# Performance work log

Hardware: AMD Instinct MI355X
Metric: run time of the kernel (lower is better)

The kernel has to match this reference:

```python
import jax, jax.numpy as jnp
import numpy as np

NUM_RELATIONS = 8
NUM_BASES = 4
IN_CH, HID, OUT_CH = 128, 64, 64
N_NODES, N_EDGES = 50000, 500000


def rgcn_conv(x, edge_src, edge_dst, edge_type, basis, comp, root, bias):
    """PyG RGCNConv with basis decomposition and per-relation mean aggregation.
    basis: [B, in, out], comp: [R, B], root: [in, out], bias: [out].
    W_r = sum_b comp[r, b] * basis[b]; msg_e = x[src_e] @ W_{type_e};
    aggregate mean over incoming edges per (node, relation), sum over relations,
    then add root transform and bias.
    """
    n = x.shape[0]
    out_dim = basis.shape[2]
    # Project once through all bases: [N, B, out]  (cheap: B=4)
    h = jnp.einsum('ni,bio->nbo', x, basis)
    # Per-edge message: contract gathered basis features with per-edge comp coeffs
    msg = jnp.einsum('eb,ebo->eo', comp[edge_type], h[edge_src])  # [E, out]
    # Mean aggregation per (dst, relation): segment id = dst*R + relation
    seg = edge_dst * NUM_RELATIONS + edge_type
    sums = jax.ops.segment_sum(msg, seg, num_segments=n * NUM_RELATIONS)
    cnt = jax.ops.segment_sum(jnp.ones((msg.shape[0], 1), msg.dtype), seg,
                              num_segments=n * NUM_RELATIONS)
    mean = sums / jnp.maximum(cnt, 1.0)
    agg = mean.reshape(n, NUM_RELATIONS, out_dim).sum(axis=1)
    return agg + x @ root + bias


def setup_inputs() -> dict:
    key = jax.random.key(0)
    ks = jax.random.split(key, 12)
    s1 = 1.0 / np.sqrt(IN_CH)
    s2 = 1.0 / np.sqrt(HID)
    return {
        'x': jax.random.normal(ks[0], (N_NODES, IN_CH), jnp.float32),
        'edge_index': jax.random.randint(ks[1], (2, N_EDGES), 0, N_NODES, jnp.int64),
        'edge_type': jax.random.randint(ks[2], (N_EDGES,), 0, NUM_RELATIONS, jnp.int64),
        'basis1': jax.random.normal(ks[3], (NUM_BASES, IN_CH, HID), jnp.float32) * s1,
        'comp1': jax.random.normal(ks[4], (NUM_RELATIONS, NUM_BASES), jnp.float32) * 0.5,
        'root1': jax.random.normal(ks[5], (IN_CH, HID), jnp.float32) * s1,
        'bias1': jnp.zeros((HID,), jnp.float32),
        'basis2': jax.random.normal(ks[6], (NUM_BASES, HID, OUT_CH), jnp.float32) * s2,
        'comp2': jax.random.normal(ks[7], (NUM_RELATIONS, NUM_BASES), jnp.float32) * 0.5,
        'root2': jax.random.normal(ks[8], (HID, OUT_CH), jnp.float32) * s2,
        'bias2': jnp.zeros((OUT_CH,), jnp.float32),
    }


def reference(x, edge_index, edge_type, basis1, comp1, root1, bias1,
              basis2, comp2, root2, bias2):
    src, dst = edge_index[0], edge_index[1]
    h = rgcn_conv(x, src, dst, edge_type, basis1, comp1, root1, bias1)
    h = jax.nn.relu(h)
    out = rgcn_conv(h, src, dst, edge_type, basis2, comp2, root2, bias2)
    return out
```

## Files before the change

### kernel.cpp

```cpp
#include <hip/hip_runtime.h>
#include <cstddef>

#define NREL 8
#define SCAN_TILE 4096

typedef __bf16 bf16x8 __attribute__((ext_vector_type(8)));
typedef float f32x4 __attribute__((ext_vector_type(4)));

__device__ __forceinline__ unsigned f2bf_u(float f) {
    unsigned u = __float_as_uint(f);
    u += 0x7FFFu + ((u >> 16) & 1u);
    return u >> 16;
}
__device__ __forceinline__ short f2bf(float f) { return (short)f2bf_u(f); }
__device__ __forceinline__ int pack2bf(float lo, float hi) {
    return (int)(f2bf_u(lo) | (f2bf_u(hi) << 16));
}
__device__ __forceinline__ float bfval(unsigned short g) {
    return __uint_as_float((unsigned)g << 16);
}

__global__ __launch_bounds__(256) void zero_kernel(int4* __restrict__ p, int n16,
                                                   int* __restrict__ offsN, int E)
{
    int i = blockIdx.x * 256 + threadIdx.x;
    if (i < n16) p[i] = make_int4(0, 0, 0, 0);
    if (i == 0) *offsN = E;
}

template<int K>
__device__ __forceinline__ void wfrag_body(const float* __restrict__ basis,
                                           const float* __restrict__ root,
                                           const float* __restrict__ comp,
                                           short* __restrict__ Wf, int tid)
{
    constexpr int NK = K / 32;
    int lane = tid & 63, slot = tid >> 6;
    int ks = slot % NK, t = slot / NK;
    int kg = lane >> 4, lr = lane & 15;
    int k0 = ks * 32 + kg * 8;
    union { short s[8]; int4 v; } u;
#pragma unroll
    for (int e = 0; e < 8; ++e) {
        int k = k0 + e;
        float v;
        if (t < 32) {
            int rr = t >> 2, ch = (t & 3) * 16 + lr;
            v = comp[rr * 4 + 0] * basis[((size_t)0 * K + k) * 64 + ch]
              + comp[rr * 4 + 1] * basis[((size_t)1 * K + k) * 64 + ch]
              + comp[rr * 4 + 2] * basis[((size_t)2 * K + k) * 64 + ch]
              + comp[rr * 4 + 3] * basis[((size_t)3 * K + k) * 64 + ch];
        } else {
            v = root[(size_t)k * 64 + (t - 32) * 16 + lr];
        }
        u.s[e] = f2bf(v);
    }
    *(int4*)(Wf + (size_t)tid * 8) = u.v;
}

__device__ __forceinline__ void afrag_body128(const float* __restrict__ x,
                                              short* __restrict__ xf, int N, int tid)
{
    int lane = tid & 63, slot = tid >> 6;
    int ks = slot & 3, rt = slot >> 2;
    int kg = lane >> 4, lr = lane & 15;
    int row = rt * 16 + lr, k = ks * 32 + kg * 8;
    union { short s[8]; int4 v; } u;
    if (row < N) {
        const float* xp = x + (size_t)row * 128 + k;
        float4 a = *(const float4*)xp;
        float4 b = *(const float4*)(xp + 4);
        u.s[0] = f2bf(a.x); u.s[1] = f2bf(a.y); u.s[2] = f2bf(a.z); u.s[3] = f2bf(a.w);
        u.s[4] = f2bf(b.x); u.s[5] = f2bf(b.y); u.s[6] = f2bf(b.z); u.s[7] = f2bf(b.w);
    } else {
        u.v = make_int4(0, 0, 0, 0);
    }
    *(int4*)(xf + (size_t)tid * 8) = u.v;
}

__global__ __launch_bounds__(256) void prep_hist_kernel(
    const int* __restrict__ dstp, const int* __restrict__ et, int* __restrict__ cnt8,
    const float* __restrict__ basis1, const float* __restrict__ root1,
    const float* __restrict__ comp1,  const float* __restrict__ basis2,
    const float* __restrict__ root2,  const float* __restrict__ comp2,
    const float* __restrict__ x,
    short* __restrict__ Wf1, short* __restrict__ Wf2, short* __restrict__ xf1,
    int E, int N, int NT, int HB)
{
    int b = blockIdx.x;
    if (b < HB) {
        int e = b * 256 + threadIdx.x;
        if (e < E) atomicAdd(&cnt8[dstp[e] * NREL + et[e]], 1);
        return;
    }
    b -= HB;
    if (b < 36) { wfrag_body<128>(basis1, root1, comp1, Wf1, b * 256 + threadIdx.x); return; }
    b -= 36;
    if (b < 18) { wfrag_body<64>(basis2, root2, comp2, Wf2, b * 256 + threadIdx.x); return; }
    b -= 18;
    int tid = b * 256 + threadIdx.x;
    if (tid < NT * 256) afrag_body128(x, xf1, N, tid);
}

__global__ __launch_bounds__(256) void scan_part(const int* __restrict__ cnt8,
                                                 int* __restrict__ tsum, int n)
{
    int base = blockIdx.x * SCAN_TILE;
    int s = 0;
    for (int i = threadIdx.x; i < SCAN_TILE; i += 256) {
        int idx = base + i;
        if (idx < n) {
            int4 a = ((const int4*)cnt8)[idx * 2];
            int4 b = ((const int4*)cnt8)[idx * 2 + 1];
            s += a.x + a.y + a.z + a.w + b.x + b.y + b.z + b.w;
        }
    }
    for (int d = 1; d < 64; d <<= 1) s += __shfl_xor(s, d, 64);
    __shared__ int ws[4];
    if ((threadIdx.x & 63) == 0) ws[threadIdx.x >> 6] = s;
    __syncthreads();
    if (threadIdx.x == 0) tsum[blockIdx.x] = ws[0] + ws[1] + ws[2] + ws[3];
}

__global__ __launch_bounds__(256) void scan_final(const int* __restrict__ cnt8,
                                                  const int* __restrict__ tsum,
                                                  int* __restrict__ offs, int n)
{
    const int lane = threadIdx.x & 63, wid = threadIdx.x >> 6;
    int tbase = 0;
    for (int i = 0; i < blockIdx.x; ++i) tbase += tsum[i];
    int base = blockIdx.x * SCAN_TILE + threadIdx.x * 16;
    int v[16]; int s = 0;
#pragma unroll
    for (int j = 0; j < 16; ++j) {
        int idx = base + j;
        int dv = 0;
        if (idx < n) {
            int4 a = ((const int4*)cnt8)[idx * 2];
            int4 b = ((const int4*)cnt8)[idx * 2 + 1];
            dv = a.x + a.y + a.z + a.w + b.x + b.y + b.z + b.w;
        }
        v[j] = dv; s += dv;
    }
    int inc = s;
    for (int d = 1; d < 64; d <<= 1) {
        int t = __shfl_up(inc, d, 64);
        if (lane >= d) inc += t;
    }
    __shared__ int wsum[4];
    if (lane == 63) wsum[wid] = inc;
    __syncthreads();
    int run = tbase + (inc - s);
    for (int k = 0; k < wid; ++k) run += wsum[k];
#pragma unroll
    for (int j = 0; j < 16; ++j) {
        int idx = base + j;
        if (idx < n) offs[idx] = run;
        run += v[j];
    }
}

template<int K>
__device__ __forceinline__ void gemm_body(const short* __restrict__ xf,
                                          const short* __restrict__ Wf,
                                          const float* __restrict__ bias,
                                          short* __restrict__ hr,
                                          short* __restrict__ yb,
                                          int N, int bx, int by)
{
    constexpr int NK = K / 32;
    const int w = threadIdx.x >> 6, lane = threadIdx.x & 63;
    const int kg = lane >> 4, lr = lane & 15;
    const int rt = bx * 4 + w;
    const int g0 = by * 3;

    bf16x8 afrag[NK];
    const short* ap = xf + ((size_t)rt * NK * 64 + lane) * 8;
#pragma unroll
    for (int ks = 0; ks < NK; ++ks)
        afrag[ks] = *(const bf16x8*)(ap + ks * 512);

    f32x4 acc[12];
#pragma unroll
    for (int t = 0; t < 12; ++t) acc[t] = (f32x4){0.f, 0.f, 0.f, 0.f};

    const short* bp = Wf + ((size_t)g0 * 4 * NK * 64 + lane) * 8;
#pragma unroll
    for (int tt = 0; tt < 12; ++tt) {
#pragma unroll
        for (int ks = 0; ks < NK; ++ks) {
            bf16x8 bfrag = *(const bf16x8*)(bp + (size_t)(tt * NK + ks) * 512);
            acc[tt] = __builtin_amdgcn_mfma_f32_16x16x32_bf16(afrag[ks], bfrag,
                                                              acc[tt], 0, 0, 0);
        }
    }

    float b0 = bias[lr], b1 = bias[16 + lr], b2 = bias[32 + lr], b3 = bias[48 + lr];

    const int drow0 = rt * 16 + kg * 4;
#pragma unroll
    for (int r = 0; r < 4; ++r) {
        int dr = drow0 + r;
        if (dr >= N) break;
#pragma unroll
        for (int gg = 0; gg < 3; ++gg) {
            int g = g0 + gg;
            if (g < 8) {
                int u0 = pack2bf(acc[gg * 4 + 0][r], acc[gg * 4 + 1][r]);
                int u1 = pack2bf(acc[gg * 4 + 2][r], acc[gg * 4 + 3][r]);
                *(int2*)(hr + (size_t)dr * 512 + g * 64 + lr * 4) = make_int2(u0, u1);
            } else {
                int u0 = pack2bf(acc[gg * 4 + 0][r] + b0, acc[gg * 4 + 1][r] + b1);
                int u1 = pack2bf(acc[gg * 4 + 2][r] + b2, acc[gg * 4 + 3][r] + b3);
                *(int2*)(yb + (size_t)dr * 64 + lr * 4) = make_int2(u0, u1);
            }
        }
    }
}

__global__ __launch_bounds__(256) void scatter_gemm1_kernel(
    const int* __restrict__ src, const int* __restrict__ dstp,
    const int* __restrict__ et,  const int* __restrict__ offs,
    int* __restrict__ cursor,    const int* __restrict__ cnt8,
    int2* __restrict__ edgeP,    int E, int SB,
    const short* __restrict__ xf1, const short* __restrict__ Wf1,
    const float* __restrict__ bias1, short* __restrict__ hr,
    short* __restrict__ yb, int N, int gblk)
{
    if (blockIdx.x < SB) {
        int e = blockIdx.x * 256 + threadIdx.x;
        if (e >= E) return;
        int d = dstp[e], r = et[e], s = src[e];
        int c = cnt8[d * NREL + r];
        float inv = 1.0f / (float)(c > 1 ? c : 1);
        int pos = offs[d] + atomicAdd(&cursor[d], 1);
        edgeP[pos] = make_int2(s * NREL + r, __float_as_int(inv));
        return;
    }
    int b = blockIdx.x - SB;
    gemm_body<128>(xf1, Wf1, bias1, hr, yb, N, b % gblk, b / gblk);
}

__global__ __launch_bounds__(256) void gemm2_kernel(const short* __restrict__ xf,
                                                    const short* __restrict__ Wf,
                                                    const float* __restrict__ bias,
                                                    short* __restrict__ hr,
                                                    short* __restrict__ yb, int N)
{
    gemm_body<64>(xf, Wf, bias, hr, yb, N, blockIdx.x, blockIdx.y);
}

template<bool BF16OUT>
__global__ __launch_bounds__(256) void agg_kernel(const int* __restrict__ offs,
                                                  const int2* __restrict__ edgeP,
                                                  const short* __restrict__ hr,
                                                  const short* __restrict__ yb,
                                                  float* __restrict__ outF,
                                                  short* __restrict__ outB, int N)
{
    __shared__ float red[2][64];
    const int w = threadIdx.x >> 6, l = threadIdx.x & 63;
    const int ds = w >> 1, sub = w & 1;
    const int dst = blockIdx.x * 2 + ds;

    const unsigned short* hp = (const unsigned short*)hr;
    float acc = 0.f;
    if (dst < N) {
        int e0 = offs[dst], e1 = offs[dst + 1];
        int e = e0 + sub;
        for (; e + 2 < e1; e += 4) {
            int2 p0 = edgeP[e], p1 = edgeP[e + 2];
            unsigned short g0 = hp[(size_t)p0.x * 64 + l];
            unsigned short g1 = hp[(size_t)p1.x * 64 + l];
            acc = fmaf(bfval(g0), __int_as_float(p0.y), acc);
            acc = fmaf(bfval(g1), __int_as_float(p1.y), acc);
        }
        if (e < e1) {
            int2 p0 = edgeP[e];
            unsigned short g0 = hp[(size_t)p0.x * 64 + l];
            acc = fmaf(bfval(g0), __int_as_float(p0.y), acc);
        }
    }
    if (sub == 1) red[ds][l] = acc;
    __syncthreads();
    if (sub == 1 || dst >= N) return;

    acc += red[ds][l];
    acc += bfval(((const unsigned short*)yb)[(size_t)dst * 64 + l]);

    int tc = (l & 3) * 16 + (l >> 2);
    if (BF16OUT) {
        int rt2 = dst >> 4, lr2 = dst & 15;
        int ks2 = tc >> 5, kg2 = (tc >> 3) & 3, e2 = tc & 7;
        outB[(((size_t)rt2 * 2 + ks2) * 64 + kg2 * 16 + lr2) * 8 + e2] =
            f2bf(fmaxf(acc, 0.f));
    } else {
        outF[(size_t)dst * 64 + tc] = acc;
    }
}

extern "C" void kernel_launch(void* const* d_in, const int* in_sizes, int n_in,
                              void* d_out, int out_size, void* d_ws, size_t ws_size,
                              hipStream_t stream)
{
    const float* x      = (const float*)d_in[0];
    const int*   ei     = (const int*)d_in[1];
    const int*   et     = (const int*)d_in[2];
    const float* basis1 = (const float*)d_in[3];
    const float* comp1  = (const float*)d_in[4];
    const float* root1  = (const float*)d_in[5];
    const float* bias1  = (const float*)d_in[6];
    const float* basis2 = (const float*)d_in[7];
    const float* comp2  = (const float*)d_in[8];
    const float* root2  = (const float*)d_in[9];
    const float* bias2  = (const float*)d_in[10];
    float* out = (float*)d_out;

    const int N = in_sizes[0] / 128;
    const int E = in_sizes[2];
    const int* src  = ei;
    const int* dstp = ei + E;

    const int gblk = (N + 63) / 64;
    const int NT   = gblk * 4;
    const int HB   = (E + 255) / 256;

    char* p = (char*)d_ws;
    auto carve = [&](size_t bytes) -> char* {
        char* q = p; p += (bytes + 255) & ~(size_t)255; return q;
    };
    int*   cursor  = (int*)carve((size_t)N * 4);
    int*   cnt8    = (int*)carve((size_t)N * NREL * 4);
    char*  zend    = p;
    int*   offs    = (int*)carve((size_t)(N + 1) * 4);
    int*   tsum    = (int*)carve(256 * 4);
    int2*  edgeP   = (int2*)carve((size_t)E * 8);
    short* Wf1     = (short*)carve((size_t)36 * 4 * 64 * 8 * 2);
    short* Wf2     = (short*)carve((size_t)36 * 2 * 64 * 8 * 2);
    short* yb      = (short*)carve((size_t)N * 64 * 2);
    short* xf1     = (short*)carve((size_t)NT * 4 * 64 * 8 * 2);
    short* xf2     = (short*)carve((size_t)NT * 2 * 64 * 8 * 2);
    short* hr      = (short*)carve((size_t)N * 512 * 2);

    const int zn16 = (int)((zend - (char*)cursor) / 16);
    const int ntiles = (N + SCAN_TILE - 1) / SCAN_TILE;

    zero_kernel<<<(zn16 + 255) / 256, 256, 0, stream>>>((int4*)cursor, zn16, offs + N, E);

    prep_hist_kernel<<<HB + 36 + 18 + NT, 256, 0, stream>>>(
        dstp, et, cnt8, basis1, root1, comp1, basis2, root2, comp2, x,
        Wf1, Wf2, xf1, E, N, NT, HB);

    scan_part<<<ntiles, 256, 0, stream>>>(cnt8, tsum, N);
    scan_final<<<ntiles, 256, 0, stream>>>(cnt8, tsum, offs, N);

    scatter_gemm1_kernel<<<HB + gblk * 3, 256, 0, stream>>>(
        src, dstp, et, offs, cursor, cnt8, edgeP, E, HB,
        xf1, Wf1, bias1, hr, yb, N, gblk);

    agg_kernel<true><<<(N + 1) / 2, 256, 0, stream>>>(offs, edgeP, hr, yb,
                                                      nullptr, xf2, N);

    gemm2_kernel<<<dim3(gblk, 3), 256, 0, stream>>>(xf2, Wf2, bias2, hr, yb, N);

    agg_kernel<false><<<(N + 1) / 2, 256, 0, stream>>>(offs, edgeP, hr, yb,
                                                       out, nullptr, N);
}
```

Baseline: 206.6 us.

## Stage GEMM weights in LDS with persistent blocks, split scatter, unroll aggregation

The GEMM kernel now loads its weight slice into LDS once per block and loops persistently over row tiles, so B fragments are no longer re-read from global memory for every tile. The scatter phase is split back into its own kernel instead of sharing a launch with GEMM1, which removes that overlap. The aggregation loop is unrolled to four gathers per iteration to expose more memory-level parallelism. LDS use (up to 48KB for K=128) may limit occupancy, and losing the scatter/GEMM overlap adds a serial launch.

```diff
diff --git a/kernel.cpp b/kernel.cpp
--- a/kernel.cpp
+++ b/kernel.cpp
@@ -160,94 +160,92 @@
     }
 }
 
+__global__ __launch_bounds__(256) void scatter_kernel(const int* __restrict__ src,
+                                                      const int* __restrict__ dst,
+                                                      const int* __restrict__ et,
+                                                      const int* __restrict__ offs,
+                                                      int* __restrict__ cursor,
+                                                      const int* __restrict__ cnt8,
+                                                      int2* __restrict__ edgeP, int E)
+{
+    int e = blockIdx.x * 256 + threadIdx.x;
+    if (e >= E) return;
+    int d = dst[e], r = et[e], s = src[e];
+    int c = cnt8[d * NREL + r];
+    float inv = 1.0f / (float)(c > 1 ? c : 1);
+    int pos = offs[d] + atomicAdd(&cursor[d], 1);
+    edgeP[pos] = make_int2(s * NREL + r, __float_as_int(inv));
+}
+
 template<int K>
-__device__ __forceinline__ void gemm_body(const short* __restrict__ xf,
-                                          const short* __restrict__ Wf,
-                                          const float* __restrict__ bias,
-                                          short* __restrict__ hr,
-                                          short* __restrict__ yb,
-                                          int N, int bx, int by)
+__global__ __launch_bounds__(256) void gemm_mfma(const short* __restrict__ xf,
+                                                 const short* __restrict__ Wf,
+                                                 const float* __restrict__ bias,
+                                                 short* __restrict__ hr,
+                                                 short* __restrict__ yb,
+                                                 int N, int gblk)
 {
     constexpr int NK = K / 32;
+    __shared__ short lds[12 * NK * 512];
+
     const int w = threadIdx.x >> 6, lane = threadIdx.x & 63;
     const int kg = lane >> 4, lr = lane & 15;
-    const int rt = bx * 4 + w;
-    const int g0 = by * 3;
-
-    bf16x8 afrag[NK];
-    const short* ap = xf + ((size_t)rt * NK * 64 + lane) * 8;
-#pragma unroll
-    for (int ks = 0; ks < NK; ++ks)
-        afrag[ks] = *(const bf16x8*)(ap + ks * 512);
-
-    f32x4 acc[12];
-#pragma unroll
-    for (int t = 0; t < 12; ++t) acc[t] = (f32x4){0.f, 0.f, 0.f, 0.f};
-
-    const short* bp = Wf + ((size_t)g0 * 4 * NK * 64 + lane) * 8;
-#pragma unroll
-    for (int tt = 0; tt < 12; ++tt) {
-#pragma unroll
-        for (int ks = 0; ks < NK; ++ks) {
-            bf16x8 bfrag = *(const bf16x8*)(bp + (size_t)(tt * NK + ks) * 512);
-            acc[tt] = __builtin_amdgcn_mfma_f32_16x16x32_bf16(afrag[ks], bfrag,
-                                                              acc[tt], 0, 0, 0);
-        }
+    const int g0 = blockIdx.y * 3;
+
+    {
+        const int4* gsrc = (const int4*)(Wf + (size_t)g0 * 4 * NK * 512);
+        int4* ldst = (int4*)lds;
+        for (int i = threadIdx.x; i < 12 * NK * 64; i += 256)
+            ldst[i] = gsrc[i];
     }
 
     float b0 = bias[lr], b1 = bias[16 + lr], b2 = bias[32 + lr], b3 = bias[48 + lr];
 
-    const int drow0 = rt * 16 + kg * 4;
-#pragma unroll
-    for (int r = 0; r < 4; ++r) {
-        int dr = drow0 + r;
-        if (dr >= N) break;
-#pragma unroll
-        for (int gg = 0; gg < 3; ++gg) {
-            int g = g0 + gg;
-            if (g < 8) {
-                int u0 = pack2bf(acc[gg * 4 + 0][r], acc[gg * 4 + 1][r]);
-                int u1 = pack2bf(acc[gg * 4 + 2][r], acc[gg * 4 + 3][r]);
-                *(int2*)(hr + (size_t)dr * 512 + g * 64 + lr * 4) = make_int2(u0, u1);
-            } else {
-                int u0 = pack2bf(acc[gg * 4 + 0][r] + b0, acc[gg * 4 + 1][r] + b1);
-                int u1 = pack2bf(acc[gg * 4 + 2][r] + b2, acc[gg * 4 + 3][r] + b3);
-                *(int2*)(yb + (size_t)dr * 64 + lr * 4) = make_int2(u0, u1);
+    __syncthreads();
+
+    for (int bx = blockIdx.x; bx < gblk; bx += gridDim.x) {
+        const int rt = bx * 4 + w;
+
+        bf16x8 afrag[NK];
+        const short* ap = xf + ((size_t)rt * NK * 64 + lane) * 8;
+#pragma unroll
+        for (int ks = 0; ks < NK; ++ks)
+            afrag[ks] = *(const bf16x8*)(ap + ks * 512);
+
+        f32x4 acc[12];
+#pragma unroll
+        for (int t = 0; t < 12; ++t) acc[t] = (f32x4){0.f, 0.f, 0.f, 0.f};
+
+#pragma unroll
+        for (int tt = 0; tt < 12; ++tt) {
+#pragma unroll
+            for (int ks = 0; ks < NK; ++ks) {
+                bf16x8 bfrag = *(const bf16x8*)(lds + (tt * NK + ks) * 512 + lane * 8);
+                acc[tt] = __builtin_amdgcn_mfma_f32_16x16x32_bf16(afrag[ks], bfrag,
+                                                                  acc[tt], 0, 0, 0);
             }
         }
-    }
-}
-
-__global__ __launch_bounds__(256) void scatter_gemm1_kernel(
-    const int* __restrict__ src, const int* __restrict__ dstp,
-    const int* __restrict__ et,  const int* __restrict__ offs,
-    int* __restrict__ cursor,    const int* __restrict__ cnt8,
-    int2* __restrict__ edgeP,    int E, int SB,
-    const short* __restrict__ xf1, const short* __restrict__ Wf1,
-    const float* __restrict__ bias1, short* __restrict__ hr,
-    short* __restrict__ yb, int N, int gblk)
-{
-    if (blockIdx.x < SB) {
-        int e = blockIdx.x * 256 + threadIdx.x;
-        if (e >= E) return;
-        int d = dstp[e], r = et[e], s = src[e];
-        int c = cnt8[d * NREL + r];
-        float inv = 1.0f / (float)(c > 1 ? c : 1);
-        int pos = offs[d] + atomicAdd(&cursor[d], 1);
-        edgeP[pos] = make_int2(s * NREL + r, __float_as_int(inv));
-        return;
-    }
-    int b = blockIdx.x - SB;
-    gemm_body<128>(xf1, Wf1, bias1, hr, yb, N, b % gblk, b / gblk);
-}
-
-__global__ __launch_bounds__(256) void gemm2_kernel(const short* __restrict__ xf,
-                                                    const short* __restrict__ Wf,
-                                                    const float* __restrict__ bias,
-                                                    short* __restrict__ hr,
-                                                    short* __restrict__ yb, int N)
-{
-    gemm_body<64>(xf, Wf, bias, hr, yb, N, blockIdx.x, blockIdx.y);
+
+        const int drow0 = rt * 16 + kg * 4;
+#pragma unroll
+        for (int r = 0; r < 4; ++r) {
+            int dr = drow0 + r;
+            if (dr >= N) break;
+#pragma unroll
+            for (int gg = 0; gg < 3; ++gg) {
+                int g = g0 + gg;
+                if (g < 8) {
+                    int u0 = pack2bf(acc[gg * 4 + 0][r], acc[gg * 4 + 1][r]);
+                    int u1 = pack2bf(acc[gg * 4 + 2][r], acc[gg * 4 + 3][r]);
+                    *(int2*)(hr + (size_t)dr * 512 + g * 64 + lr * 4) = make_int2(u0, u1);
+                } else {
+                    int u0 = pack2bf(acc[gg * 4 + 0][r] + b0, acc[gg * 4 + 1][r] + b1);
+                    int u1 = pack2bf(acc[gg * 4 + 2][r] + b2, acc[gg * 4 + 3][r] + b3);
+                    *(int2*)(yb + (size_t)dr * 64 + lr * 4) = make_int2(u0, u1);
+                }
+            }
+        }
+    }
 }
 
 template<bool BF16OUT>
@@ -268,14 +266,19 @@
     if (dst < N) {
         int e0 = offs[dst], e1 = offs[dst + 1];
         int e = e0 + sub;
-        for (; e + 2 < e1; e += 4) {
-            int2 p0 = edgeP[e], p1 = edgeP[e + 2];
+        for (; e + 6 < e1; e += 8) {
+            int2 p0 = edgeP[e],     p1 = edgeP[e + 2];
+            int2 p2 = edgeP[e + 4], p3 = edgeP[e + 6];
             unsigned short g0 = hp[(size_t)p0.x * 64 + l];
             unsigned short g1 = hp[(size_t)p1.x * 64 + l];
+            unsigned short g2 = hp[(size_t)p2.x * 64 + l];
+            unsigned short g3 = hp[(size_t)p3.x * 64 + l];
             acc = fmaf(bfval(g0), __int_as_float(p0.y), acc);
             acc = fmaf(bfval(g1), __int_as_float(p1.y), acc);
-        }
-        if (e < e1) {
+            acc = fmaf(bfval(g2), __int_as_float(p2.y), acc);
+            acc = fmaf(bfval(g3), __int_as_float(p3.y), acc);
+        }
+        for (; e < e1; e += 2) {
             int2 p0 = edgeP[e];
             unsigned short g0 = hp[(size_t)p0.x * 64 + l];
             acc = fmaf(bfval(g0), __int_as_float(p0.y), acc);
@@ -354,14 +357,15 @@
     scan_part<<<ntiles, 256, 0, stream>>>(cnt8, tsum, N);
     scan_final<<<ntiles, 256, 0, stream>>>(cnt8, tsum, offs, N);
 
-    scatter_gemm1_kernel<<<HB + gblk * 3, 256, 0, stream>>>(
-        src, dstp, et, offs, cursor, cnt8, edgeP, E, HB,
-        xf1, Wf1, bias1, hr, yb, N, gblk);
+    scatter_kernel<<<HB, 256, 0, stream>>>(src, dstp, et, offs, cursor,
+                                           cnt8, edgeP, E);
+
+    gemm_mfma<128><<<dim3(256, 3), 256, 0, stream>>>(xf1, Wf1, bias1, hr, yb, N, gblk);
 
     agg_kernel<true><<<(N + 1) / 2, 256, 0, stream>>>(offs, edgeP, hr, yb,
                                                       nullptr, xf2, N);
 
-    gemm2_kernel<<<dim3(gblk, 3), 256, 0, stream>>>(xf2, Wf2, bias2, hr, yb, N);
+    gemm_mfma<64><<<dim3(512, 3), 256, 0, stream>>>(xf2, Wf2, bias2, hr, yb, N, gblk);
 
     agg_kernel<false><<<(N + 1) / 2, 256, 0, stream>>>(offs, edgeP, hr, yb,
                                                        out, nullptr, N);
```

Result: no change. 208.7 us (+1.0%).
